# Optimization experiments

Measured on AMD Instinct MI355X. Metric: run time of the kernel, lower is better.

## Reference

```python
import jax, jax.numpy as jnp
import numpy as np

N = 8192        # num nodes (bs in the original docstring)
D_IN = 512      # input feature dim
HEADS = 8
DPH = 512 // HEADS  # size_per_head = hidden_size // num_heads
EDGE_P = 0.01   # adjacency density


def setup_inputs() -> dict:
    key = jax.random.key(0)
    k1, k2, k3 = jax.random.split(key, 3)
    H = jax.random.normal(k1, (N, D_IN), dtype=jnp.float32)
    # dense 0/1 adjacency, as passed to the layer before tf.sparse.from_dense
    adj = (jax.random.uniform(k2, (N, N)) < EDGE_P).astype(jnp.float32)
    # Glorot-uniform per-head projection kernels, stacked: (HEADS, D_IN, DPH)
    limit = float(np.sqrt(6.0 / (D_IN + DPH)))
    W = jax.random.uniform(k3, (HEADS, D_IN, DPH), jnp.float32, -limit, limit)
    b = jnp.zeros((HEADS, DPH), jnp.float32)
    return {"H": H, "adj": adj, "W": W, "b": b}


def reference(H, adj, W, b):
    # Per-head dense projection: H_ = H @ W_h  -> (HEADS, N, DPH)
    H_ = jnp.einsum('nd,hde->hne', H, W)
    # NOTE: the original layer computes a sparse sigmoid/softmax attention
    # (f1 + f2^T over adj) but never uses it: head_output uses raw adj.
    # Aggregation: adj @ H_ per head, plus bias; activation = tf.identity.
    out = jnp.einsum('nm,hme->hne', adj, H_) + b[:, None, :]  # (HEADS, N, DPH)
    # Concat heads along feature axis (head 0 first) -> (N, HEADS*DPH)
    return jnp.transpose(out, (1, 0, 2)).reshape(H.shape[0], HEADS * DPH)
```

## Files before the change

### kernel.cpp

```cpp
#include <hip/hip_runtime.h>
#include <hip/hip_bf16.h>

typedef __attribute__((ext_vector_type(8))) short short8;
typedef __attribute__((ext_vector_type(4))) float floatx4;
typedef __attribute__((ext_vector_type(4))) uint uintx4;

#define GN 8192
#define GD 512
#define GEMM_BLOCKS 512

static __device__ __forceinline__ ushort bf16bits(float x) {
  __hip_bfloat16 h = __float2bfloat16(x);
  return *(ushort*)&h;
}
static __device__ __forceinline__ float bf16f(uint u16) {
  return __uint_as_float(u16 << 16);
}

typedef __attribute__((address_space(1))) const void g1_void;
typedef __attribute__((address_space(3))) void l3_void;
static __device__ __forceinline__ void gl_lds16(const void* g, void* l) {
  __builtin_amdgcn_global_load_lds((g1_void*)g, (l3_void*)l, 16, 0, 0);
}

__global__ void detect_kernel(const uint* __restrict__ H, const uint* __restrict__ W,
                              const uint* __restrict__ adj, const uint* __restrict__ b,
                              int* __restrict__ flags, float* __restrict__ bias) {
  __shared__ int cH, cW, cA, cB;
  const int t = threadIdx.x;
  if (t == 0) { cH = 0; cW = 0; cA = 0; cB = 0; }
  __syncthreads();
  { const uint e = (H[t] >> 7) & 0xFFu; if (e >= 100u && e <= 140u) atomicAdd(&cH, 1); }
  { const uint e = (W[t] >> 7) & 0xFFu; if (e >= 100u && e <= 140u) atomicAdd(&cW, 1); }
  for (int i = t; i < 4096; i += 256)
    if ((adj[i] & 0xFFFFu) == 0x3F80u) atomicAdd(&cA, 1);
  if (b[t] != 0u) atomicAdd(&cB, 1);
  __syncthreads();
  const int hb = cH > 128, wb = cW > 128, ab = cA > 0;
  if (t == 0) { flags[0] = hb; flags[1] = wb; flags[2] = ab; }
  if (cB == 0) {
    bias[t] = 0.0f; bias[t + 256] = 0.0f;
  } else if (wb) {
    const ushort* bs = (const ushort*)b;
    bias[t] = bf16f(bs[t]); bias[t + 256] = bf16f(bs[t + 256]);
  } else {
    const float* bf = (const float*)b;
    bias[t] = bf[t]; bias[t + 256] = bf[t + 256];
  }
}

#define BM 128
#define BN 64
#define BK 64
#define LDK 72

#define SMEM_BYTES (BM * LDK * 2 + BN * LDK * 2)

__global__ __launch_bounds__(256) void proj_kernel(
    const void* __restrict__ Hv, const void* __restrict__ Wv,
    ushort* __restrict__ HPt, const int* __restrict__ flags) {
  __shared__ __align__(16) unsigned char smem[SMEM_BYTES];
  ushort* sA = (ushort*)smem;
  ushort* sB = (ushort*)(smem + BM * LDK * 2);
  const int tid = threadIdx.x;
  const int hb = flags[0];
  const int wb = flags[1];
  const int bn = blockIdx.x & 7;
  const int bm = blockIdx.x >> 3;
  const int m0 = bm * BM;
  const int lane = tid & 63;
  const int w = tid >> 6;
  const int wr = w >> 1, wc = w & 1;
  const int l15 = lane & 15, q = lane >> 4;

  floatx4 acc[4][2];
#pragma unroll
  for (int i = 0; i < 4; i++)
#pragma unroll
    for (int j = 0; j < 2; j++) acc[i][j] = (floatx4)0.0f;

  for (int k0 = 0; k0 < GD; k0 += BK) {
    __syncthreads();
    if (hb) {
      const ushort* H16 = (const ushort*)Hv;
      const int r = tid >> 3;
      const int kc = (tid & 7) * 8;
#pragma unroll
      for (int p = 0; p < 4; p++) {
        const int row = r + p * 32;
        const uint4 v = *(const uint4*)(H16 + (size_t)(m0 + row) * GD + k0 + kc);
        *(uint4*)(sA + row * LDK + kc) = v;
      }
    } else {
      const float* H32 = (const float*)Hv;
      const int r0 = tid >> 4;
      const int kc = (tid & 15) * 4;
#pragma unroll
      for (int p = 0; p < 8; p++) {
        const int row = r0 + p * 16;
        const float4 v = *(const float4*)(H32 + (size_t)(m0 + row) * GD + k0 + kc);
        ushort4 o;
        o.x = bf16bits(v.x); o.y = bf16bits(v.y);
        o.z = bf16bits(v.z); o.w = bf16bits(v.w);
        *(ushort4*)(sA + row * LDK + kc) = o;
      }
    }
    if (wb) {
      const ushort* Wh = (const ushort*)Wv + (size_t)bn * (512 * 64);
      const int kk = tid >> 3;
      const int e0 = (tid & 7) * 8;
#pragma unroll
      for (int p = 0; p < 2; p++) {
        const int k = kk + p * 32;
        const uint4 v = *(const uint4*)(Wh + (size_t)(k0 + k) * 64 + e0);
        const ushort* pv = (const ushort*)&v;
#pragma unroll
        for (int j = 0; j < 8; j++) sB[(e0 + j) * LDK + k] = pv[j];
      }
    } else {
      const float* Wh = (const float*)Wv + (size_t)bn * (512 * 64);
      const int kk = tid >> 4;
      const int e0 = (tid & 15) * 4;
#pragma unroll
      for (int p = 0; p < 4; p++) {
        const int k = kk + p * 16;
        const float4 v = *(const float4*)(Wh + (size_t)(k0 + k) * 64 + e0);
        sB[(e0 + 0) * LDK + k] = bf16bits(v.x);
        sB[(e0 + 1) * LDK + k] = bf16bits(v.y);
        sB[(e0 + 2) * LDK + k] = bf16bits(v.z);
        sB[(e0 + 3) * LDK + k] = bf16bits(v.w);
      }
    }
    __syncthreads();
#pragma unroll
    for (int kq = 0; kq < 2; kq++) {
      short8 af[4], bfv[2];
#pragma unroll
      for (int mt = 0; mt < 4; mt++)
        af[mt] = *(const short8*)(sA + (wr * 64 + mt * 16 + l15) * LDK + kq * 32 + q * 8);
#pragma unroll
      for (int ct = 0; ct < 2; ct++)
        bfv[ct] = *(const short8*)(sB + (wc * 32 + ct * 16 + l15) * LDK + kq * 32 + q * 8);
#pragma unroll
      for (int mt = 0; mt < 4; mt++)
#pragma unroll
        for (int ct = 0; ct < 2; ct++)
          acc[mt][ct] = __builtin_amdgcn_mfma_f32_16x16x32_bf16(
              af[mt], bfv[ct], acc[mt][ct], 0, 0, 0);
    }
  }
#pragma unroll
  for (int mt = 0; mt < 4; mt++)
#pragma unroll
    for (int ct = 0; ct < 2; ct++) {
      const int col = bn * 64 + wc * 32 + ct * 16 + l15;
      const int rowb = m0 + wr * 64 + mt * 16 + q * 4;
      ushort4 o;
      o.x = bf16bits(acc[mt][ct][0]);
      o.y = bf16bits(acc[mt][ct][1]);
      o.z = bf16bits(acc[mt][ct][2]);
      o.w = bf16bits(acc[mt][ct][3]);
      *(ushort4*)(HPt + (size_t)col * GN + rowb) = o;
    }
}

#define ABM 64
#define ABK 64
#define AKCH 2048
#define ALDA 72

__global__ __launch_bounds__(512) void agg_kernel(
    const void* __restrict__ adjv, const ushort* __restrict__ HPt,
    float* __restrict__ pbuf, const int* __restrict__ flags) {
  __shared__ __align__(16) ushort sA[ABM * ALDA];
  __shared__ __align__(16) ushort sB[GD * 64];
  const int ab = flags[2];
  const int bid = blockIdx.x;
  const int kch = bid & 3;
  const int m0 = (bid >> 2) * ABM;
  const size_t kb = (size_t)kch * AKCH;
  const int tid = threadIdx.x;
  const int lane = tid & 63, w = tid >> 6;
  const int l15 = lane & 15, q = lane >> 4;

  floatx4 acc[4][4];
#pragma unroll
  for (int i = 0; i < 4; i++)
#pragma unroll
    for (int j = 0; j < 4; j++) acc[i][j] = (floatx4)0.0f;

  const int brow = lane >> 3;
  const int bkc = ((lane & 7) ^ brow) * 8;

  for (int k0 = 0; k0 < AKCH; k0 += ABK) {
    __syncthreads();
#pragma unroll
    for (int p = 0; p < 8; p++) {
      const int e = p * 64 + w * 8 + brow;
      gl_lds16(HPt + (size_t)e * GN + kb + k0 + bkc,
               sB + (size_t)(p * 64 + w * 8) * 64);
    }
    if (ab) {
      const ushort* adj16 = (const ushort*)adjv;
      const int n = tid >> 3;
      const int kc = (tid & 7) * 8;
      const uintx4 v = __builtin_nontemporal_load(
          (const uintx4*)(adj16 + (size_t)(m0 + n) * GN + kb + k0 + kc));
      *(uintx4*)(sA + n * ALDA + kc) = v;
    } else {
      const float* adj32 = (const float*)adjv;
      const int n = tid >> 3;
      const int kc = (tid & 7) * 8;
      const float* src = adj32 + (size_t)(m0 + n) * GN + kb + k0 + kc;
      const floatx4 v0 = __builtin_nontemporal_load((const floatx4*)src);
      const floatx4 v1 = __builtin_nontemporal_load((const floatx4*)(src + 4));
      ushort4 o0, o1;
      o0.x = bf16bits(v0.x); o0.y = bf16bits(v0.y);
      o0.z = bf16bits(v0.z); o0.w = bf16bits(v0.w);
      o1.x = bf16bits(v1.x); o1.y = bf16bits(v1.y);
      o1.z = bf16bits(v1.z); o1.w = bf16bits(v1.w);
      *(ushort4*)(sA + n * ALDA + kc) = o0;
      *(ushort4*)(sA + n * ALDA + kc + 4) = o1;
    }
    __syncthreads();
#pragma unroll
    for (int kq = 0; kq < 2; kq++) {
      short8 af[4], bfr[4];
#pragma unroll
      for (int mt = 0; mt < 4; mt++)
        af[mt] = *(const short8*)(sA + (mt * 16 + l15) * ALDA + kq * 32 + q * 8);
#pragma unroll
      for (int ct = 0; ct < 4; ct++) {
        const int r = w * 64 + ct * 16 + l15;
        const int slot = (kq * 4 + q) ^ (l15 & 7);
        bfr[ct] = *(const short8*)(sB + r * 64 + slot * 8);
      }
#pragma unroll
      for (int mt = 0; mt < 4; mt++)
#pragma unroll
        for (int ct = 0; ct < 4; ct++)
          acc[mt][ct] = __builtin_amdgcn_mfma_f32_16x16x32_bf16(
              af[mt], bfr[ct], acc[mt][ct], 0, 0, 0);
    }
  }
  float* pb = pbuf + (size_t)kch * ((size_t)GN * GD);
#pragma unroll
  for (int mt = 0; mt < 4; mt++)
#pragma unroll
    for (int ct = 0; ct < 4; ct++) {
      const int col = w * 64 + ct * 16 + l15;
      const int rowb = m0 + mt * 16 + q * 4;
#pragma unroll
      for (int r = 0; r < 4; r++)
        __builtin_nontemporal_store(
            acc[mt][ct][r], pb + (size_t)(rowb + r) * GD + col);
    }
}

__global__ __launch_bounds__(256) void combine_kernel(
    const float* __restrict__ pbuf, const float* __restrict__ bias,
    float* __restrict__ out) {
  const int i = blockIdx.x * 256 + threadIdx.x;
  const size_t stride = (size_t)GN * GD / 4;
  floatx4 s = __builtin_nontemporal_load((const floatx4*)pbuf + i);
#pragma unroll
  for (int j = 1; j < 4; j++) {
    const floatx4 a = __builtin_nontemporal_load(
        (const floatx4*)pbuf + j * stride + i);
    s.x += a.x; s.y += a.y; s.z += a.z; s.w += a.w;
  }
  const floatx4 bb = *((const floatx4*)bias + (i & 127));
  floatx4 o;
  o.x = s.x + bb.x; o.y = s.y + bb.y; o.z = s.z + bb.z; o.w = s.w + bb.w;
  __builtin_nontemporal_store(o, (floatx4*)out + i);
}

extern "C" void kernel_launch(void* const* d_in, const int* in_sizes, int n_in,
                              void* d_out, int out_size, void* d_ws, size_t ws_size,
                              hipStream_t stream) {
  const void *H = d_in[0], *adj = d_in[1], *W = d_in[2], *b = d_in[3];
  for (int i = 0; i < n_in; i++) {
    const int s = in_sizes[i];
    if (s == GN * GN) adj = d_in[i];
    else if (s == GN * GD) H = d_in[i];
    else if (s == 8 * 512 * 64) W = d_in[i];
    else if (s == 512) b = d_in[i];
  }
  float* out = (float*)d_out;

  char* ws = (char*)d_ws;
  ushort* HPt  = (ushort*)ws;
  float*  bias = (float*)(ws + (size_t)GN * GD * 2);
  int*    flags= (int*)(ws + (size_t)GN * GD * 2 + 4096);
  float*  pbuf = (float*)(ws + (size_t)16 * 1024 * 1024);

  detect_kernel<<<1, 256, 0, stream>>>((const uint*)H, (const uint*)W,
                                       (const uint*)adj, (const uint*)b,
                                       flags, bias);
  proj_kernel<<<GEMM_BLOCKS, 256, 0, stream>>>(H, W, HPt, flags);
  agg_kernel<<<512, 512, 0, stream>>>(adj, HPt, pbuf, flags);
  combine_kernel<<<4096, 256, 0, stream>>>(pbuf, bias, out);
}
```

Before: 514.1 us.

## Double-buffer aggregation tiles and halve split-K partitions

The aggregation kernel now double-buffers the projected-feature tile in LDS and prefetches the next adjacency tile into registers while MFMAs run on the current one, so global loads overlap compute. The K split drops from 4 to 2 chunks, with 256 blocks each covering 4096 columns. The combine kernel therefore reduces 2 partial buffers instead of 4, cutting partial-sum traffic. In exchange, LDS use roughly doubles, there are two barriers per iteration, and with half the blocks on a 256-CU part each CU may hold only one block.

```diff
diff --git a/kernel.cpp b/kernel.cpp
--- a/kernel.cpp
+++ b/kernel.cpp
@@ -166,63 +166,90 @@
 
 #define ABM 64
 #define ABK 64
-#define AKCH 2048
+#define AKCH 4096
+#define ANT (AKCH / ABK)
 #define ALDA 72
 
-__global__ __launch_bounds__(512) void agg_kernel(
+__global__ __launch_bounds__(512, 2) void agg_kernel(
     const void* __restrict__ adjv, const ushort* __restrict__ HPt,
     float* __restrict__ pbuf, const int* __restrict__ flags) {
   __shared__ __align__(16) ushort sA[ABM * ALDA];
-  __shared__ __align__(16) ushort sB[GD * 64];
+  __shared__ __align__(16) ushort sB[2][GD * 64];
   const int ab = flags[2];
   const int bid = blockIdx.x;
-  const int kch = bid & 3;
-  const int m0 = (bid >> 2) * ABM;
+  const int kch = bid & 1;
+  const int m0 = (bid >> 1) * ABM;
   const size_t kb = (size_t)kch * AKCH;
   const int tid = threadIdx.x;
   const int lane = tid & 63, w = tid >> 6;
   const int l15 = lane & 15, q = lane >> 4;
 
-  floatx4 acc[4][4];
-#pragma unroll
-  for (int i = 0; i < 4; i++)
-#pragma unroll
-    for (int j = 0; j < 4; j++) acc[i][j] = (floatx4)0.0f;
-
   const int brow = lane >> 3;
   const int bkc = ((lane & 7) ^ brow) * 8;
-
-  for (int k0 = 0; k0 < AKCH; k0 += ABK) {
-    __syncthreads();
-#pragma unroll
-    for (int p = 0; p < 8; p++) {
-      const int e = p * 64 + w * 8 + brow;
-      gl_lds16(HPt + (size_t)e * GN + kb + k0 + bkc,
-               sB + (size_t)(p * 64 + w * 8) * 64);
-    }
-    if (ab) {
-      const ushort* adj16 = (const ushort*)adjv;
-      const int n = tid >> 3;
-      const int kc = (tid & 7) * 8;
-      const uintx4 v = __builtin_nontemporal_load(
-          (const uintx4*)(adj16 + (size_t)(m0 + n) * GN + kb + k0 + kc));
-      *(uintx4*)(sA + n * ALDA + kc) = v;
-    } else {
-      const float* adj32 = (const float*)adjv;
-      const int n = tid >> 3;
-      const int kc = (tid & 7) * 8;
-      const float* src = adj32 + (size_t)(m0 + n) * GN + kb + k0 + kc;
-      const floatx4 v0 = __builtin_nontemporal_load((const floatx4*)src);
-      const floatx4 v1 = __builtin_nontemporal_load((const floatx4*)(src + 4));
-      ushort4 o0, o1;
-      o0.x = bf16bits(v0.x); o0.y = bf16bits(v0.y);
-      o0.z = bf16bits(v0.z); o0.w = bf16bits(v0.w);
-      o1.x = bf16bits(v1.x); o1.y = bf16bits(v1.y);
-      o1.z = bf16bits(v1.z); o1.w = bf16bits(v1.w);
-      *(ushort4*)(sA + n * ALDA + kc) = o0;
-      *(ushort4*)(sA + n * ALDA + kc + 4) = o1;
-    }
-    __syncthreads();
+  const int an = tid >> 3;
+  const int akc = (tid & 7) * 8;
+
+  const ushort* adj16 = (const ushort*)adjv;
+  const float* adj32 = (const float*)adjv;
+
+  floatx4 acc[4][4];
+#pragma unroll
+  for (int i = 0; i < 4; i++)
+#pragma unroll
+    for (int j = 0; j < 4; j++) acc[i][j] = (floatx4)0.0f;
+
+  floatx4 a0, a1;
+  uintx4 au;
+
+#define STAGE_B(K0, BUF)                                                  \
+  {                                                                       \
+    _Pragma("unroll")                                                     \
+    for (int p = 0; p < 8; p++) {                                         \
+      const int e = p * 64 + w * 8 + brow;                                \
+      gl_lds16(HPt + (size_t)e * GN + kb + (K0) + bkc,                    \
+               &sB[BUF][(p * 64 + w * 8) * 64]);                          \
+    }                                                                     \
+  }
+
+#define LOAD_A(K0)                                                        \
+  {                                                                       \
+    if (ab) {                                                             \
+      au = __builtin_nontemporal_load(                                    \
+          (const uintx4*)(adj16 + (size_t)(m0 + an) * GN + kb + (K0) + akc)); \
+    } else {                                                              \
+      const float* src = adj32 + (size_t)(m0 + an) * GN + kb + (K0) + akc;\
+      a0 = __builtin_nontemporal_load((const floatx4*)src);               \
+      a1 = __builtin_nontemporal_load((const floatx4*)(src + 4));         \
+    }                                                                     \
+  }
+
+#define WRITE_A()                                                         \
+  {                                                                       \
+    if (ab) {                                                             \
+      *(uintx4*)(sA + an * ALDA + akc) = au;                              \
+    } else {                                                              \
+      ushort4 o0, o1;                                                     \
+      o0.x = bf16bits(a0.x); o0.y = bf16bits(a0.y);                       \
+      o0.z = bf16bits(a0.z); o0.w = bf16bits(a0.w);                       \
+      o1.x = bf16bits(a1.x); o1.y = bf16bits(a1.y);                       \
+      o1.z = bf16bits(a1.z); o1.w = bf16bits(a1.w);                       \
+      *(ushort4*)(sA + an * ALDA + akc) = o0;                             \
+      *(ushort4*)(sA + an * ALDA + akc + 4) = o1;                        \
+    }                                                                     \
+  }
+
+  STAGE_B(0, 0)
+  LOAD_A(0)
+  WRITE_A()
+  __syncthreads();
+
+  int cur = 0;
+  for (int k = 0; k < ANT; ++k) {
+    const int k1 = (k + 1) * ABK;
+    if (k + 1 < ANT) {
+      STAGE_B(k1, cur ^ 1)
+      LOAD_A(k1)
+    }
 #pragma unroll
     for (int kq = 0; kq < 2; kq++) {
       short8 af[4], bfr[4];
@@ -233,7 +260,7 @@
       for (int ct = 0; ct < 4; ct++) {
         const int r = w * 64 + ct * 16 + l15;
         const int slot = (kq * 4 + q) ^ (l15 & 7);
-        bfr[ct] = *(const short8*)(sB + r * 64 + slot * 8);
+        bfr[ct] = *(const short8*)(&sB[cur][r * 64 + slot * 8]);
       }
 #pragma unroll
       for (int mt = 0; mt < 4; mt++)
@@ -242,7 +269,12 @@
           acc[mt][ct] = __builtin_amdgcn_mfma_f32_16x16x32_bf16(
               af[mt], bfr[ct], acc[mt][ct], 0, 0, 0);
     }
-  }
+    __syncthreads();
+    if (k + 1 < ANT) WRITE_A()
+    __syncthreads();
+    cur ^= 1;
+  }
+
   float* pb = pbuf + (size_t)kch * ((size_t)GN * GD);
 #pragma unroll
   for (int mt = 0; mt < 4; mt++)
@@ -255,6 +287,9 @@
         __builtin_nontemporal_store(
             acc[mt][ct][r], pb + (size_t)(rowb + r) * GD + col);
     }
+#undef STAGE_B
+#undef LOAD_A
+#undef WRITE_A
 }
 
 __global__ __launch_bounds__(256) void combine_kernel(
@@ -262,16 +297,14 @@
     float* __restrict__ out) {
   const int i = blockIdx.x * 256 + threadIdx.x;
   const size_t stride = (size_t)GN * GD / 4;
-  floatx4 s = __builtin_nontemporal_load((const floatx4*)pbuf + i);
-#pragma unroll
-  for (int j = 1; j < 4; j++) {
-    const floatx4 a = __builtin_nontemporal_load(
-        (const floatx4*)pbuf + j * stride + i);
-    s.x += a.x; s.y += a.y; s.z += a.z; s.w += a.w;
-  }
+  const floatx4 p0 = __builtin_nontemporal_load((const floatx4*)pbuf + i);
+  const floatx4 p1 = __builtin_nontemporal_load((const floatx4*)pbuf + stride + i);
   const floatx4 bb = *((const floatx4*)bias + (i & 127));
   floatx4 o;
-  o.x = s.x + bb.x; o.y = s.y + bb.y; o.z = s.z + bb.z; o.w = s.w + bb.w;
+  o.x = p0.x + p1.x + bb.x;
+  o.y = p0.y + p1.y + bb.y;
+  o.z = p0.z + p1.z + bb.z;
+  o.w = p0.w + p1.w + bb.w;
   __builtin_nontemporal_store(o, (floatx4*)out + i);
 }
 
@@ -298,6 +331,6 @@
                                        (const uint*)adj, (const uint*)b,
                                        flags, bias);
   proj_kernel<<<GEMM_BLOCKS, 256, 0, stream>>>(H, W, HPt, flags);
-  agg_kernel<<<512, 512, 0, stream>>>(adj, HPt, pbuf, flags);
+  agg_kernel<<<256, 512, 0, stream>>>(adj, HPt, pbuf, flags);
   combine_kernel<<<4096, 256, 0, stream>>>(pbuf, bias, out);
 }
```

Measured after the change: 501.0 us. -2.5%, faster.
